# Performance work log

Measured on AMD Instinct MI355X. Metric: run time of the kernel, lower is better.

Reference implementation:

```python
import jax, jax.numpy as jnp
import numpy as np

B, L, E = 4, 2048, 1024
H, DQ, DV = 8, 128, 128
SCALE = 1.0 / np.sqrt(DQ).astype(np.float32)


def setup_inputs() -> dict:
    key = jax.random.key(0)
    ks = jax.random.split(key, 6)
    return {
        "qInputs": jax.random.normal(ks[0], (B, L, E), dtype=jnp.float32),
        "kvInputs": jax.random.normal(ks[1], (B, L, E), dtype=jnp.float32),
        "mask": jnp.zeros((B, H, L, L), dtype=jnp.bool_),
        "W_Q": jax.random.normal(ks[2], (E, H * DQ), dtype=jnp.float32) * 0.02,
        "W_K": jax.random.normal(ks[3], (E, H * DQ), dtype=jnp.float32) * 0.02,
        "W_V": jax.random.normal(ks[4], (E, H * DV), dtype=jnp.float32) * 0.02,
        "W_fc": jax.random.normal(ks[5], (H * DV, E), dtype=jnp.float32) * 0.02,
    }


def reference(qInputs, kvInputs, mask, W_Q, W_K, W_V, W_fc):
    b, lq, _ = qInputs.shape
    lk = kvInputs.shape[1]
    # Projections -> [B, H, L, D]
    Q = (qInputs @ W_Q).reshape(b, lq, H, DQ).transpose(0, 2, 1, 3)
    K = (kvInputs @ W_K).reshape(b, lk, H, DQ).transpose(0, 2, 1, 3)
    V = (kvInputs @ W_V).reshape(b, lk, H, DV).transpose(0, 2, 1, 3)
    # Scaled dot-product with additive mask fill of -1e9
    scores = jnp.einsum("bhqd,bhkd->bhqk", Q, K) * SCALE
    scores = jnp.where(mask, jnp.float32(-1e9), scores)
    attn = jax.nn.softmax(scores, axis=-1)
    ctx = jnp.einsum("bhqk,bhkd->bhqd", attn, V)
    ctx = ctx.transpose(0, 2, 1, 3).reshape(b, lq, H * DV)
    return ctx @ W_fc
```

## Files before the change

kernel.cpp:

```cpp
#include <hip/hip_runtime.h>
#include <stdint.h>

#define LQ 2048
#define EDIM 1024
#define HN 8
#define DH 128
#define BATCH 4
#define SCALE_LOG2E 0.12753785051263942f

typedef short bf16x8 __attribute__((ext_vector_type(8)));
typedef float f32x4 __attribute__((ext_vector_type(4)));
typedef unsigned short u16;
typedef unsigned short u16x4 __attribute__((ext_vector_type(4)));

__device__ __forceinline__ u16 f2bf(float f) {
  union { float f; uint32_t u; } c; c.f = f;
  uint32_t u = c.u;
  return (u16)((u + 0x7fffu + ((u >> 16) & 1u)) >> 16);
}

__device__ __forceinline__ void async16(const void* g, void* l) {
  __builtin_amdgcn_global_load_lds((const __attribute__((address_space(1))) void*)g,
                                   (__attribute__((address_space(3))) void*)l, 16, 0, 0);
}

__device__ __forceinline__ uint32_t lds_b(const u16* p) {
  return (uint32_t)(uintptr_t)(__attribute__((address_space(3))) const u16*)p;
}
__device__ __forceinline__ void ldsr4_issue(bf16x8& d0, bf16x8& d1, bf16x8& d2, bf16x8& d3,
                                            uint32_t a0, uint32_t a1, uint32_t a2, uint32_t a3) {
  asm volatile("ds_read_b128 %0, %4\n\t"
               "ds_read_b128 %1, %5\n\t"
               "ds_read_b128 %2, %6\n\t"
               "ds_read_b128 %3, %7"
               : "=&v"(d0), "=&v"(d1), "=&v"(d2), "=&v"(d3)
               : "v"(a0), "v"(a1), "v"(a2), "v"(a3));
}
template <int N>
__device__ __forceinline__ void lgkm_wait_sb() {
  asm volatile("s_waitcnt lgkmcnt(%0)" :: "n"(N) : "memory");
  __builtin_amdgcn_sched_barrier(0);
}
__device__ __forceinline__ uint32_t cvtpk(float lo, float hi) {
  uint32_t r;
  asm("v_cvt_pk_bf16_f32 %0, %1, %2" : "=v"(r) : "v"(lo), "v"(hi));
  return r;
}
__device__ __forceinline__ void plane_swap(uint32_t& a, uint32_t& b) {
#if __has_builtin(__builtin_amdgcn_permlane32_swap) && __has_builtin(__builtin_amdgcn_permlane16_swap)
  auto r1 = __builtin_amdgcn_permlane32_swap(a, b, false, false);
  auto r2 = __builtin_amdgcn_permlane16_swap(r1[0], r1[1], false, false);
  a = r2[0];
  b = r2[1];
#else
  asm("s_nop 1\n\t"
      "v_permlane32_swap_b32 %0, %1\n\t"
      "s_nop 1\n\t"
      "v_permlane16_swap_b32 %0, %1\n\t"
      "s_nop 1"
      : "+v"(a), "+v"(b));
#endif
}
__device__ __forceinline__ float xorsum16(float x) {
#if __has_builtin(__builtin_amdgcn_permlane16_swap)
  union { float f; uint32_t u; } c; c.f = x;
  auto r = __builtin_amdgcn_permlane16_swap(c.u, c.u, false, false);
  union { uint32_t u; float f; } a, b; a.u = r[0]; b.u = r[1];
  return a.f + b.f;
#else
  return x + __shfl_xor(x, 16);
#endif
}
__device__ __forceinline__ float xorsum32(float x) {
#if __has_builtin(__builtin_amdgcn_permlane32_swap)
  union { float f; uint32_t u; } c; c.f = x;
  auto r = __builtin_amdgcn_permlane32_swap(c.u, c.u, false, false);
  union { uint32_t u; float f; } a, b; a.u = r[0]; b.u = r[1];
  return a.f + b.f;
#else
  return x + __shfl_xor(x, 32);
#endif
}

__global__ __launch_bounds__(256) void prep_kernel(const float* __restrict__ qIn, const float* __restrict__ kvIn,
                                                   const float* __restrict__ w0, const float* __restrict__ w1,
                                                   const float* __restrict__ w2, const float* __restrict__ w3,
                                                   u16* __restrict__ oq, u16* __restrict__ okv,
                                                   u16* __restrict__ o0, u16* __restrict__ o1,
                                                   u16* __restrict__ o2, u16* __restrict__ o3) {
  __shared__ float tile[32][33];
  const int bid = blockIdx.x;
  const int t = threadIdx.x;
  if (bid < 16384) {
    const float* in = (bid >= 8192) ? kvIn : qIn;
    u16* out = (bid >= 8192) ? okv : oq;
    size_t i = (size_t)(bid & 8191) * 256 + t;
    float4 v = ((const float4*)in)[i];
    u16x4 o;
    o.x = f2bf(v.x); o.y = f2bf(v.y); o.z = f2bf(v.z); o.w = f2bf(v.w);
    ((u16x4*)out)[i] = o;
  } else {
    const int idx = bid - 16384;
    const int z = idx >> 10;
    const int rem = idx & 1023;
    const float* in; u16* out;
    switch (z) {
      case 0: in = w0; out = o0; break;
      case 1: in = w1; out = o1; break;
      case 2: in = w2; out = o2; break;
      default: in = w3; out = o3; break;
    }
    const int tx = t & 31, ty = t >> 5;
    const int x0 = (rem & 31) * 32;
    const int y0 = (rem >> 5) * 32;
#pragma unroll
    for (int j = 0; j < 32; j += 8)
      tile[ty + j][tx] = in[(size_t)(y0 + ty + j) * EDIM + x0 + tx];
    __syncthreads();
#pragma unroll
    for (int j = 0; j < 32; j += 8)
      out[(size_t)(x0 + ty + j) * EDIM + (y0 + tx)] = f2bf(tile[tx][ty + j]);
  }
}

struct GemmCore {
  template <typename EpiF>
  static __device__ __forceinline__ void run(const u16* __restrict__ A, const u16* __restrict__ Bt,
                                             int m0, int n0, u16* As, u16* Bs, EpiF epi) {
    const int tid = threadIdx.x;
    const int l = tid & 63;
    const int w = tid >> 6;
    const int wm = (w >> 1) * 64;
    const int wn = (w & 1) * 64;
    const int fm = l & 15;
    const int q4 = l >> 4;
    const int f7 = fm & 7;
    f32x4 acc[4][4] = {};
    for (int k0 = 0; k0 < EDIM; k0 += 64) {
      __syncthreads();
#pragma unroll
      for (int ii = 0; ii < 4; ++ii) {
        const int rloc = w * 32 + ii * 8 + (l >> 3);
        const int cs = (l & 7) ^ (rloc & 7);
        async16(A + (size_t)(m0 + rloc) * EDIM + k0 + cs * 8, &As[(w * 32 + ii * 8) * 64 + l * 8]);
        async16(Bt + (size_t)(n0 + rloc) * EDIM + k0 + cs * 8, &Bs[(w * 32 + ii * 8) * 64 + l * 8]);
      }
      __syncthreads();
#pragma unroll
      for (int ks = 0; ks < 2; ++ks) {
        const int coff = ((ks * 4 + q4) ^ f7) * 8;
        bf16x8 a[4], b[4];
#pragma unroll
        for (int i = 0; i < 4; ++i) a[i] = *(const bf16x8*)&As[(wm + i * 16 + fm) * 64 + coff];
#pragma unroll
        for (int j = 0; j < 4; ++j) b[j] = *(const bf16x8*)&Bs[(wn + j * 16 + fm) * 64 + coff];
#pragma unroll
        for (int i = 0; i < 4; ++i)
#pragma unroll
          for (int j = 0; j < 4; ++j)
            acc[i][j] = __builtin_amdgcn_mfma_f32_16x16x32_bf16(a[i], b[j], acc[i][j], 0, 0, 0);
      }
    }
    const int rr = q4 * 4;
#pragma unroll
    for (int i = 0; i < 4; ++i)
#pragma unroll
      for (int j = 0; j < 4; ++j)
#pragma unroll
        for (int r = 0; r < 4; ++r)
          epi(m0 + wm + i * 16 + rr + r, n0 + wn + j * 16 + fm, acc[i][j][r]);
  }
};

__global__ __launch_bounds__(256) void qkv_gemm(const u16* __restrict__ xq, const u16* __restrict__ xkv,
                                                const u16* __restrict__ WqT, const u16* __restrict__ WkT,
                                                const u16* __restrict__ WvT,
                                                u16* __restrict__ Qb, u16* __restrict__ Kb,
                                                u16* __restrict__ Vt,
                                                const unsigned char* __restrict__ mask,
                                                unsigned char* __restrict__ flags) {
  __shared__ __align__(16) u16 As[128 * 64];
  __shared__ __align__(16) u16 Bs[128 * 64];
  __shared__ int wany[4];
  const int z = blockIdx.z;
  if (z == 3) {
    const int t = threadIdx.x;
    const int unit0 = (blockIdx.x * 8 + blockIdx.y) * 16;
#pragma unroll 1
    for (int u = 0; u < 16; ++u) {
      const int idx = unit0 + u;
      const int bh = idx >> 8;
      const int tile16 = idx & 255;
      const int qt = tile16 >> 4, kt = tile16 & 15;
      const int r = t >> 1;
      const size_t base = ((size_t)bh * LQ + qt * 128 + r) * LQ + kt * 128 + (t & 1) * 64;
      const uint4* p = (const uint4*)(mask + base);
      uint4 a = p[0], c = p[1], d = p[2], e = p[3];
      uint32_t any = a.x | a.y | a.z | a.w | c.x | c.y | c.z | c.w |
                     d.x | d.y | d.z | d.w | e.x | e.y | e.z | e.w;
      int wa = __any(any != 0);
      if ((t & 63) == 0) wany[t >> 6] = wa;
      __syncthreads();
      if (t == 0)
        flags[(size_t)bh * 256 + tile16] = (unsigned char)(wany[0] | wany[1] | wany[2] | wany[3]);
      __syncthreads();
    }
    return;
  }
  if (z == 0) {
    GemmCore::run(xq, WqT, blockIdx.x * 128, blockIdx.y * 128, As, Bs,
                  [&](int gm, int gn, float v) { Qb[(size_t)gm * EDIM + gn] = f2bf(v * SCALE_LOG2E); });
  } else if (z == 1) {
    GemmCore::run(xkv, WkT, blockIdx.x * 128, blockIdx.y * 128, As, Bs,
                  [&](int gm, int gn, float v) { Kb[(size_t)gm * EDIM + gn] = f2bf(v); });
  } else {
    GemmCore::run(WvT, xkv, blockIdx.y * 128, blockIdx.x * 128, As, Bs,
                  [&](int gm, int gn, float v) {
                    Vt[((size_t)(gn >> 11) * 1024 + gm) * 2048 + (gn & 2047)] = f2bf(v);
                  });
  }
}

__global__ __launch_bounds__(256) void out_gemm(const u16* __restrict__ ctx, const u16* __restrict__ WfcT,
                                                float* __restrict__ out) {
  __shared__ __align__(16) u16 As[128 * 64];
  __shared__ __align__(16) u16 Bs[128 * 64];
  GemmCore::run(ctx, WfcT, blockIdx.x * 128, blockIdx.y * 128, As, Bs,
                [&](int gm, int gn, float v) { out[(size_t)gm * EDIM + gn] = v; });
}

__global__ __launch_bounds__(256, 2) void attn_kernel(const u16* __restrict__ Qb, const u16* __restrict__ Kb,
                                                      const u16* __restrict__ Vt,
                                                      const unsigned char* __restrict__ mask,
                                                      const unsigned char* __restrict__ flags,
                                                      u16* __restrict__ ctx) {
  __shared__ __align__(16) u16 Ktile[2][64 * 128];
  __shared__ __align__(16) u16 Vtile[2][128 * 64];
  const int tid = threadIdx.x;
  const int l = tid & 63;
  const int w = tid >> 6;
  const int flat = blockIdx.x;
  const int xcd = flat & 7;
  const int idx = flat >> 3;
  const int panel = xcd * 4 + (idx >> 4);
  const int qt = idx & 15;
  const int h = panel & 7;
  const int b = panel >> 3;
  const int fm = l & 15;
  const int q4 = l >> 4;
  const int fk = q4 * 8;
  const int f7 = fm & 7;
  const int qbase = qt * 128 + w * 32;
  const int bh = b * HN + h;

  const u16* Kbh = Kb + (size_t)b * LQ * EDIM + h * DH;
  const u16* Vth = Vt + (size_t)bh * DH * LQ;
  const size_t mbase = (size_t)bh * (size_t)LQ * LQ;

  const unsigned char* tf = flags + (size_t)bh * 256 + qt * 16;
  uint32_t fmask = 0;
#pragma unroll
  for (int i = 0; i < 16; ++i) fmask |= (tf[i] ? 1u : 0u) << i;

  bf16x8 qf[2][4];
#pragma unroll
  for (int mt = 0; mt < 2; ++mt)
#pragma unroll
    for (int ks = 0; ks < 4; ++ks)
      qf[mt][ks] = *(const bf16x8*)(Qb + (size_t)(b * LQ + qbase + mt * 16 + fm) * EDIM + h * DH + ks * 32 + fk);

  auto stageK = [&](int kt_, int buf) {
#pragma unroll
    for (int ii = 0; ii < 4; ++ii) {
      const int i = w * 4 + ii;
      const int row = i * 4 + (l >> 4);
      const int g = (l & 15) ^ (row & 7);
      async16(Kbh + (size_t)(kt_ * 64 + row) * EDIM + g * 8, &Ktile[buf][i * 512 + l * 8]);
    }
  };
  auto stageV = [&](int kt_, int buf) {
#pragma unroll
    for (int ii = 0; ii < 4; ++ii) {
      const int i = w * 4 + ii;
      const int row = i * 8 + (l >> 3);
      const int g = (l & 7) ^ (row & 7);
      async16(Vth + (size_t)row * LQ + kt_ * 64 + g * 8, &Vtile[buf][i * 512 + l * 8]);
    }
  };

  stageK(0, 0);
  stageV(0, 0);

  f32x4 o[2][8] = {};
  float lsumv[2] = {0.f, 0.f};

  for (int it = 0; it < 32; ++it) {
    const int cur = it & 1;
    __syncthreads();
    if (it + 1 < 32) { stageK(it + 1, 1 - cur); stageV(it + 1, 1 - cur); }

    const u16* KT = &Ktile[cur][0];
    const u16* VT = &Vtile[cur][0];

    f32x4 st[4][2] = {};
    bf16x8 kf[2][4];
    bf16x8 v0, v1, v2, v3, v4, v5, v6, v7;
    bf16x8 x0, x1, x2, x3, x4, x5, x6, x7;
    {
      const int slot = q4 ^ f7;
      ldsr4_issue(kf[0][0], kf[0][1], kf[0][2], kf[0][3],
                  lds_b(KT + (0 * 16 + fm) * 128 + slot * 8),
                  lds_b(KT + (1 * 16 + fm) * 128 + slot * 8),
                  lds_b(KT + (2 * 16 + fm) * 128 + slot * 8),
                  lds_b(KT + (3 * 16 + fm) * 128 + slot * 8));
    }
#pragma unroll
    for (int ks = 0; ks < 3; ++ks) {
      const int c = ks & 1;
      const int slot = ((ks + 1) * 4 + q4) ^ f7;
      ldsr4_issue(kf[c ^ 1][0], kf[c ^ 1][1], kf[c ^ 1][2], kf[c ^ 1][3],
                  lds_b(KT + (0 * 16 + fm) * 128 + slot * 8),
                  lds_b(KT + (1 * 16 + fm) * 128 + slot * 8),
                  lds_b(KT + (2 * 16 + fm) * 128 + slot * 8),
                  lds_b(KT + (3 * 16 + fm) * 128 + slot * 8));
      lgkm_wait_sb<4>();
      __builtin_amdgcn_s_setprio(1);
#pragma unroll
      for (int mt = 0; mt < 2; ++mt) {
        st[0][mt] = __builtin_amdgcn_mfma_f32_16x16x32_bf16(kf[c][0], qf[mt][ks], st[0][mt], 0, 0, 0);
        st[1][mt] = __builtin_amdgcn_mfma_f32_16x16x32_bf16(kf[c][1], qf[mt][ks], st[1][mt], 0, 0, 0);
        st[2][mt] = __builtin_amdgcn_mfma_f32_16x16x32_bf16(kf[c][2], qf[mt][ks], st[2][mt], 0, 0, 0);
        st[3][mt] = __builtin_amdgcn_mfma_f32_16x16x32_bf16(kf[c][3], qf[mt][ks], st[3][mt], 0, 0, 0);
      }
      __builtin_amdgcn_s_setprio(0);
    }
    {
      const int vs0 = q4 ^ f7;
      ldsr4_issue(v0, v1, v2, v3,
                  lds_b(VT + (0 * 16 + fm) * 64 + vs0 * 8), lds_b(VT + (1 * 16 + fm) * 64 + vs0 * 8),
                  lds_b(VT + (2 * 16 + fm) * 64 + vs0 * 8), lds_b(VT + (3 * 16 + fm) * 64 + vs0 * 8));
      ldsr4_issue(v4, v5, v6, v7,
                  lds_b(VT + (4 * 16 + fm) * 64 + vs0 * 8), lds_b(VT + (5 * 16 + fm) * 64 + vs0 * 8),
                  lds_b(VT + (6 * 16 + fm) * 64 + vs0 * 8), lds_b(VT + (7 * 16 + fm) * 64 + vs0 * 8));
      lgkm_wait_sb<8>();
      __builtin_amdgcn_s_setprio(1);
#pragma unroll
      for (int mt = 0; mt < 2; ++mt) {
        st[0][mt] = __builtin_amdgcn_mfma_f32_16x16x32_bf16(kf[1][0], qf[mt][3], st[0][mt], 0, 0, 0);
        st[1][mt] = __builtin_amdgcn_mfma_f32_16x16x32_bf16(kf[1][1], qf[mt][3], st[1][mt], 0, 0, 0);
        st[2][mt] = __builtin_amdgcn_mfma_f32_16x16x32_bf16(kf[1][2], qf[mt][3], st[2][mt], 0, 0, 0);
        st[3][mt] = __builtin_amdgcn_mfma_f32_16x16x32_bf16(kf[1][3], qf[mt][3], st[3][mt], 0, 0, 0);
      }
      __builtin_amdgcn_s_setprio(0);
    }

    const int hasMask = (fmask >> (it >> 1)) & 1;
    uint32_t pk[2][4][2];
    float sA[2], sB[2];
    bf16x8 paf0, paf1;
#pragma unroll
    for (int mt = 0; mt < 2; ++mt) {
      float sum = 0.f;
      if (hasMask) {
        const unsigned char* mrow = mask + mbase + (size_t)(qbase + mt * 16 + fm) * LQ + it * 64 + q4 * 4;
#pragma unroll
        for (int kt = 0; kt < 2; ++kt) {
          const uint32_t mv = *(const uint32_t*)(mrow + kt * 16);
#pragma unroll
          for (int r = 0; r < 4; ++r) {
            float e = ((mv >> (8 * r)) & 0xffu) ? 0.f : exp2f(st[kt][mt][r]);
            st[kt][mt][r] = e;
            sum += e;
          }
        }
      } else {
#pragma unroll
        for (int kt = 0; kt < 2; ++kt)
#pragma unroll
          for (int r = 0; r < 4; ++r) {
            float e = exp2f(st[kt][mt][r]);
            st[kt][mt][r] = e;
            sum += e;
          }
      }
      sA[mt] = sum;
      pk[mt][0][0] = cvtpk(st[0][mt][0], st[0][mt][1]);
      pk[mt][0][1] = cvtpk(st[0][mt][2], st[0][mt][3]);
      pk[mt][1][0] = cvtpk(st[1][mt][0], st[1][mt][1]);
      pk[mt][1][1] = cvtpk(st[1][mt][2], st[1][mt][3]);
    }
    {
      union { uint32_t u[4]; bf16x8 v; } fb;
      uint32_t e0 = pk[0][0][0], f0 = pk[0][1][0];
      uint32_t e1 = pk[0][0][1], f1 = pk[0][1][1];
      plane_swap(e0, f0); plane_swap(e1, f1);
      fb.u[0] = e0; fb.u[1] = e1; fb.u[2] = f0; fb.u[3] = f1;
      paf0 = fb.v;
      uint32_t g0 = pk[1][0][0], h0 = pk[1][1][0];
      uint32_t g1 = pk[1][0][1], h1 = pk[1][1][1];
      plane_swap(g0, h0); plane_swap(g1, h1);
      fb.u[0] = g0; fb.u[1] = g1; fb.u[2] = h0; fb.u[3] = h1;
      paf1 = fb.v;
    }
    {
      const int vs1 = (4 + q4) ^ f7;
      ldsr4_issue(x0, x1, x2, x3,
                  lds_b(VT + (0 * 16 + fm) * 64 + vs1 * 8), lds_b(VT + (1 * 16 + fm) * 64 + vs1 * 8),
                  lds_b(VT + (2 * 16 + fm) * 64 + vs1 * 8), lds_b(VT + (3 * 16 + fm) * 64 + vs1 * 8));
      ldsr4_issue(x4, x5, x6, x7,
                  lds_b(VT + (4 * 16 + fm) * 64 + vs1 * 8), lds_b(VT + (5 * 16 + fm) * 64 + vs1 * 8),
                  lds_b(VT + (6 * 16 + fm) * 64 + vs1 * 8), lds_b(VT + (7 * 16 + fm) * 64 + vs1 * 8));
    }
    lgkm_wait_sb<8>();
    __builtin_amdgcn_s_setprio(1);
    o[0][0] = __builtin_amdgcn_mfma_f32_16x16x32_bf16(paf0, v0, o[0][0], 0, 0, 0);
    o[1][0] = __builtin_amdgcn_mfma_f32_16x16x32_bf16(paf1, v0, o[1][0], 0, 0, 0);
    o[0][1] = __builtin_amdgcn_mfma_f32_16x16x32_bf16(paf0, v1, o[0][1], 0, 0, 0);
    o[1][1] = __builtin_amdgcn_mfma_f32_16x16x32_bf16(paf1, v1, o[1][1], 0, 0, 0);
    o[0][2] = __builtin_amdgcn_mfma_f32_16x16x32_bf16(paf0, v2, o[0][2], 0, 0, 0);
    o[1][2] = __builtin_amdgcn_mfma_f32_16x16x32_bf16(paf1, v2, o[1][2], 0, 0, 0);
    o[0][3] = __builtin_amdgcn_mfma_f32_16x16x32_bf16(paf0, v3, o[0][3], 0, 0, 0);
    o[1][3] = __builtin_amdgcn_mfma_f32_16x16x32_bf16(paf1, v3, o[1][3], 0, 0, 0);
    o[0][4] = __builtin_amdgcn_mfma_f32_16x16x32_bf16(paf0, v4, o[0][4], 0, 0, 0);
    o[1][4] = __builtin_amdgcn_mfma_f32_16x16x32_bf16(paf1, v4, o[1][4], 0, 0, 0);
    o[0][5] = __builtin_amdgcn_mfma_f32_16x16x32_bf16(paf0, v5, o[0][5], 0, 0, 0);
    o[1][5] = __builtin_amdgcn_mfma_f32_16x16x32_bf16(paf1, v5, o[1][5], 0, 0, 0);
    o[0][6] = __builtin_amdgcn_mfma_f32_16x16x32_bf16(paf0, v6, o[0][6], 0, 0, 0);
    o[1][6] = __builtin_amdgcn_mfma_f32_16x16x32_bf16(paf1, v6, o[1][6], 0, 0, 0);
    o[0][7] = __builtin_amdgcn_mfma_f32_16x16x32_bf16(paf0, v7, o[0][7], 0, 0, 0);
    o[1][7] = __builtin_amdgcn_mfma_f32_16x16x32_bf16(paf1, v7, o[1][7], 0, 0, 0);
    __builtin_amdgcn_s_setprio(0);

#pragma unroll
    for (int mt = 0; mt < 2; ++mt) {
      float sum = 0.f;
      if (hasMask) {
        const unsigned char* mrow = mask + mbase + (size_t)(qbase + mt * 16 + fm) * LQ + it * 64 + q4 * 4;
#pragma unroll
        for (int kt = 2; kt < 4; ++kt) {
          const uint32_t mv = *(const uint32_t*)(mrow + kt * 16);
#pragma unroll
          for (int r = 0; r < 4; ++r) {
            float e = ((mv >> (8 * r)) & 0xffu) ? 0.f : exp2f(st[kt][mt][r]);
            st[kt][mt][r] = e;
            sum += e;
          }
        }
      } else {
#pragma unroll
        for (int kt = 2; kt < 4; ++kt)
#pragma unroll
          for (int r = 0; r < 4; ++r) {
            float e = exp2f(st[kt][mt][r]);
            st[kt][mt][r] = e;
            sum += e;
          }
      }
      sB[mt] = sum;
      pk[mt][2][0] = cvtpk(st[2][mt][0], st[2][mt][1]);
      pk[mt][2][1] = cvtpk(st[2][mt][2], st[2][mt][3]);
      pk[mt][3][0] = cvtpk(st[3][mt][0], st[3][mt][1]);
      pk[mt][3][1] = cvtpk(st[3][mt][2], st[3][mt][3]);
    }
    {
      union { uint32_t u[4]; bf16x8 v; } fb;
      uint32_t e0 = pk[0][2][0], f0 = pk[0][3][0];
      uint32_t e1 = pk[0][2][1], f1 = pk[0][3][1];
      plane_swap(e0, f0); plane_swap(e1, f1);
      fb.u[0] = e0; fb.u[1] = e1; fb.u[2] = f0; fb.u[3] = f1;
      paf0 = fb.v;
      uint32_t g0 = pk[1][2][0], h0 = pk[1][3][0];
      uint32_t g1 = pk[1][2][1], h1 = pk[1][3][1];
      plane_swap(g0, h0); plane_swap(g1, h1);
      fb.u[0] = g0; fb.u[1] = g1; fb.u[2] = h0; fb.u[3] = h1;
      paf1 = fb.v;
    }
#pragma unroll
    for (int mt = 0; mt < 2; ++mt) {
      float t = sA[mt] + sB[mt];
      lsumv[mt] += xorsum32(xorsum16(t));
    }

    lgkm_wait_sb<0>();
    __builtin_amdgcn_s_setprio(1);
    o[0][0] = __builtin_amdgcn_mfma_f32_16x16x32_bf16(paf0, x0, o[0][0], 0, 0, 0);
    o[1][0] = __builtin_amdgcn_mfma_f32_16x16x32_bf16(paf1, x0, o[1][0], 0, 0, 0);
    o[0][1] = __builtin_amdgcn_mfma_f32_16x16x32_bf16(paf0, x1, o[0][1], 0, 0, 0);
    o[1][1] = __builtin_amdgcn_mfma_f32_16x16x32_bf16(paf1, x1, o[1][1], 0, 0, 0);
    o[0][2] = __builtin_amdgcn_mfma_f32_16x16x32_bf16(paf0, x2, o[0][2], 0, 0, 0);
    o[1][2] = __builtin_amdgcn_mfma_f32_16x16x32_bf16(paf1, x2, o[1][2], 0, 0, 0);
    o[0][3] = __builtin_amdgcn_mfma_f32_16x16x32_bf16(paf0, x3, o[0][3], 0, 0, 0);
    o[1][3] = __builtin_amdgcn_mfma_f32_16x16x32_bf16(paf1, x3, o[1][3], 0, 0, 0);
    o[0][4] = __builtin_amdgcn_mfma_f32_16x16x32_bf16(paf0, x4, o[0][4], 0, 0, 0);
    o[1][4] = __builtin_amdgcn_mfma_f32_16x16x32_bf16(paf1, x4, o[1][4], 0, 0, 0);
    o[0][5] = __builtin_amdgcn_mfma_f32_16x16x32_bf16(paf0, x5, o[0][5], 0, 0, 0);
    o[1][5] = __builtin_amdgcn_mfma_f32_16x16x32_bf16(paf1, x5, o[1][5], 0, 0, 0);
    o[0][6] = __builtin_amdgcn_mfma_f32_16x16x32_bf16(paf0, x6, o[0][6], 0, 0, 0);
    o[1][6] = __builtin_amdgcn_mfma_f32_16x16x32_bf16(paf1, x6, o[1][6], 0, 0, 0);
    o[0][7] = __builtin_amdgcn_mfma_f32_16x16x32_bf16(paf0, x7, o[0][7], 0, 0, 0);
    o[1][7] = __builtin_amdgcn_mfma_f32_16x16x32_bf16(paf1, x7, o[1][7], 0, 0, 0);
    __builtin_amdgcn_s_setprio(0);
  }

#pragma unroll
  for (int mt = 0; mt < 2; ++mt)
#pragma unroll
    for (int r = 0; r < 4; ++r) {
      float inv = 1.f / __shfl(lsumv[mt], q4 * 4 + r);
      int gq = b * LQ + qbase + mt * 16 + q4 * 4 + r;
#pragma unroll
      for (int dt = 0; dt < 8; ++dt)
        ctx[(size_t)gq * EDIM + h * DH + dt * 16 + fm] = f2bf(o[mt][dt][r] * inv);
    }
}

extern "C" void kernel_launch(void* const* d_in, const int* in_sizes, int n_in,
                              void* d_out, int out_size, void* d_ws, size_t ws_size,
                              hipStream_t stream) {
  const float* qIn = (const float*)d_in[0];
  const float* kvIn = (const float*)d_in[1];
  const unsigned char* mask = (const unsigned char*)d_in[2];
  const float* W_Q = (const float*)d_in[3];
  const float* W_K = (const float*)d_in[4];
  const float* W_V = (const float*)d_in[5];
  const float* W_fc = (const float*)d_in[6];
  float* out = (float*)d_out;

  uint8_t* ws = (uint8_t*)d_ws;
  const size_t MB = 1u << 20;
  u16* xq   = (u16*)(ws);
  u16* xkv  = (u16*)(ws + 16 * MB);
  u16* WqT  = (u16*)(ws + 32 * MB);
  u16* WkT  = (u16*)(ws + 34 * MB);
  u16* WvT  = (u16*)(ws + 36 * MB);
  u16* WfcT = (u16*)(ws + 38 * MB);
  u16* Qb   = (u16*)(ws + 40 * MB);
  u16* Kb   = (u16*)(ws + 56 * MB);
  u16* Vt   = (u16*)(ws + 72 * MB);
  u16* ctx  = (u16*)(ws + 88 * MB);
  unsigned char* flags = (unsigned char*)(ws + 104 * MB);

  prep_kernel<<<20480, 256, 0, stream>>>(qIn, kvIn, W_Q, W_K, W_V, W_fc,
                                         xq, xkv, WqT, WkT, WvT, WfcT);
  qkv_gemm<<<dim3(64, 8, 4), 256, 0, stream>>>(xq, xkv, WqT, WkT, WvT, Qb, Kb, Vt, mask, flags);
  attn_kernel<<<512, 256, 0, stream>>>(Qb, Kb, Vt, mask, flags, ctx);
  out_gemm<<<dim3(64, 8), 256, 0, stream>>>(ctx, WfcT, out);
}
```

Before: 826.6 us.

## Scan mask inline in attention kernel and swizzle GEMM tile order

Drops the separate mask-flag pass that rode along as an extra z-slice of the QKV GEMM. Each attention wave now reads its own 32 rows of the mask for the next 128-column tile, one tile ahead, and sets the skip decision per wave with __any. The aim is to stop reading the whole 128MB mask in a dedicated pass, overlap the mask reads with attention compute, and avoid writing and reading the flag buffer. It also remaps the 64x8 GEMM block indices through a swizzle to improve L2 reuse. Attention still reads the full mask, now inside its main loop, which could add latency.

New measurement: 812.6 us, median of 2. No clear change (-1.7%).

```diff
diff --git a/kernel.cpp b/kernel.cpp
--- a/kernel.cpp
+++ b/kernel.cpp
@@ -80,6 +80,11 @@
 #else
   return x + __shfl_xor(x, 32);
 #endif
+}
+__device__ __forceinline__ void swz64(int& x, int& y) {
+  const int f = x + 64 * y;
+  x = (f & 7) * 8 + ((f >> 3) & 7);
+  y = f >> 6;
 }
 
 __global__ __launch_bounds__(256) void prep_kernel(const float* __restrict__ qIn, const float* __restrict__ kvIn,
@@ -176,45 +181,20 @@
                                                 const u16* __restrict__ WqT, const u16* __restrict__ WkT,
                                                 const u16* __restrict__ WvT,
                                                 u16* __restrict__ Qb, u16* __restrict__ Kb,
-                                                u16* __restrict__ Vt,
-                                                const unsigned char* __restrict__ mask,
-                                                unsigned char* __restrict__ flags) {
+                                                u16* __restrict__ Vt) {
   __shared__ __align__(16) u16 As[128 * 64];
   __shared__ __align__(16) u16 Bs[128 * 64];
-  __shared__ int wany[4];
   const int z = blockIdx.z;
-  if (z == 3) {
-    const int t = threadIdx.x;
-    const int unit0 = (blockIdx.x * 8 + blockIdx.y) * 16;
-#pragma unroll 1
-    for (int u = 0; u < 16; ++u) {
-      const int idx = unit0 + u;
-      const int bh = idx >> 8;
-      const int tile16 = idx & 255;
-      const int qt = tile16 >> 4, kt = tile16 & 15;
-      const int r = t >> 1;
-      const size_t base = ((size_t)bh * LQ + qt * 128 + r) * LQ + kt * 128 + (t & 1) * 64;
-      const uint4* p = (const uint4*)(mask + base);
-      uint4 a = p[0], c = p[1], d = p[2], e = p[3];
-      uint32_t any = a.x | a.y | a.z | a.w | c.x | c.y | c.z | c.w |
-                     d.x | d.y | d.z | d.w | e.x | e.y | e.z | e.w;
-      int wa = __any(any != 0);
-      if ((t & 63) == 0) wany[t >> 6] = wa;
-      __syncthreads();
-      if (t == 0)
-        flags[(size_t)bh * 256 + tile16] = (unsigned char)(wany[0] | wany[1] | wany[2] | wany[3]);
-      __syncthreads();
-    }
-    return;
-  }
+  int bx = blockIdx.x, by = blockIdx.y;
+  swz64(bx, by);
   if (z == 0) {
-    GemmCore::run(xq, WqT, blockIdx.x * 128, blockIdx.y * 128, As, Bs,
+    GemmCore::run(xq, WqT, bx * 128, by * 128, As, Bs,
                   [&](int gm, int gn, float v) { Qb[(size_t)gm * EDIM + gn] = f2bf(v * SCALE_LOG2E); });
   } else if (z == 1) {
-    GemmCore::run(xkv, WkT, blockIdx.x * 128, blockIdx.y * 128, As, Bs,
+    GemmCore::run(xkv, WkT, bx * 128, by * 128, As, Bs,
                   [&](int gm, int gn, float v) { Kb[(size_t)gm * EDIM + gn] = f2bf(v); });
   } else {
-    GemmCore::run(WvT, xkv, blockIdx.y * 128, blockIdx.x * 128, As, Bs,
+    GemmCore::run(WvT, xkv, by * 128, bx * 128, As, Bs,
                   [&](int gm, int gn, float v) {
                     Vt[((size_t)(gn >> 11) * 1024 + gm) * 2048 + (gn & 2047)] = f2bf(v);
                   });
@@ -225,14 +205,15 @@
                                                 float* __restrict__ out) {
   __shared__ __align__(16) u16 As[128 * 64];
   __shared__ __align__(16) u16 Bs[128 * 64];
-  GemmCore::run(ctx, WfcT, blockIdx.x * 128, blockIdx.y * 128, As, Bs,
+  int bx = blockIdx.x, by = blockIdx.y;
+  swz64(bx, by);
+  GemmCore::run(ctx, WfcT, bx * 128, by * 128, As, Bs,
                 [&](int gm, int gn, float v) { out[(size_t)gm * EDIM + gn] = v; });
 }
 
 __global__ __launch_bounds__(256, 2) void attn_kernel(const u16* __restrict__ Qb, const u16* __restrict__ Kb,
                                                       const u16* __restrict__ Vt,
                                                       const unsigned char* __restrict__ mask,
-                                                      const unsigned char* __restrict__ flags,
                                                       u16* __restrict__ ctx) {
   __shared__ __align__(16) u16 Ktile[2][64 * 128];
   __shared__ __align__(16) u16 Vtile[2][128 * 64];
@@ -256,11 +237,7 @@
   const u16* Kbh = Kb + (size_t)b * LQ * EDIM + h * DH;
   const u16* Vth = Vt + (size_t)bh * DH * LQ;
   const size_t mbase = (size_t)bh * (size_t)LQ * LQ;
-
-  const unsigned char* tf = flags + (size_t)bh * 256 + qt * 16;
-  uint32_t fmask = 0;
-#pragma unroll
-  for (int i = 0; i < 16; ++i) fmask |= (tf[i] ? 1u : 0u) << i;
+  const unsigned char* mscan = mask + mbase + (size_t)(qbase + (l >> 1)) * LQ + (l & 1) * 64;
 
   bf16x8 qf[2][4];
 #pragma unroll
@@ -268,6 +245,13 @@
 #pragma unroll
     for (int ks = 0; ks < 4; ++ks)
       qf[mt][ks] = *(const bf16x8*)(Qb + (size_t)(b * LQ + qbase + mt * 16 + fm) * EDIM + h * DH + ks * 32 + fk);
+
+  uint32_t curAcc = 0, nxtAcc = 0;
+#pragma unroll
+  for (int j = 0; j < 4; ++j) {
+    uint4 mv = *(const uint4*)(mscan + j * 16);
+    curAcc |= mv.x | mv.y | mv.z | mv.w;
+  }
 
   auto stageK = [&](int kt_, int buf) {
 #pragma unroll
@@ -298,6 +282,21 @@
     const int cur = it & 1;
     __syncthreads();
     if (it + 1 < 32) { stageK(it + 1, 1 - cur); stageV(it + 1, 1 - cur); }
+
+    if ((it & 1) == 0) {
+      if (it > 0) curAcc = nxtAcc;
+      nxtAcc = 0;
+      const int tn = (it >> 1) + 1;
+      if (tn < 16) {
+        const unsigned char* ms = mscan + tn * 128;
+#pragma unroll
+        for (int j = 0; j < 4; ++j) {
+          uint4 mv = *(const uint4*)(ms + j * 16);
+          nxtAcc |= mv.x | mv.y | mv.z | mv.w;
+        }
+      }
+    }
+    const int hasMask = __any(curAcc != 0);
 
     const u16* KT = &Ktile[cur][0];
     const u16* VT = &Vtile[cur][0];
@@ -354,7 +353,6 @@
       __builtin_amdgcn_s_setprio(0);
     }
 
-    const int hasMask = (fmask >> (it >> 1)) & 1;
     uint32_t pk[2][4][2];
     float sA[2], sB[2];
     bf16x8 paf0, paf1;
@@ -538,11 +536,10 @@
   u16* Kb   = (u16*)(ws + 56 * MB);
   u16* Vt   = (u16*)(ws + 72 * MB);
   u16* ctx  = (u16*)(ws + 88 * MB);
-  unsigned char* flags = (unsigned char*)(ws + 104 * MB);
 
   prep_kernel<<<20480, 256, 0, stream>>>(qIn, kvIn, W_Q, W_K, W_V, W_fc,
                                          xq, xkv, WqT, WkT, WvT, WfcT);
-  qkv_gemm<<<dim3(64, 8, 4), 256, 0, stream>>>(xq, xkv, WqT, WkT, WvT, Qb, Kb, Vt, mask, flags);
-  attn_kernel<<<512, 256, 0, stream>>>(Qb, Kb, Vt, mask, flags, ctx);
+  qkv_gemm<<<dim3(64, 8, 3), 256, 0, stream>>>(xq, xkv, WqT, WkT, WvT, Qb, Kb, Vt);
+  attn_kernel<<<512, 256, 0, stream>>>(Qb, Kb, Vt, mask, ctx);
   out_gemm<<<dim3(64, 8), 256, 0, stream>>>(ctx, WfcT, out);
 }
```
